# Kernel tuning notes

Hardware: AMD Instinct MI355X
Metric: run time of the kernel (lower is better)

## Reference

```python
import jax, jax.numpy as jnp
import numpy as np

N = 100000
E = 2000000
F = 64          # in_features == out_features (required by attention * h_j)
BETA = 0.5
NEG_SLOPE = 0.01  # torch F.leaky_relu default


def setup_inputs() -> dict:
    key = jax.random.key(0)
    k1, k2, k3, k4, k5, k6 = jax.random.split(key, 6)
    h = jax.random.normal(k1, (N, F), dtype=jnp.float32)
    adj = jax.random.randint(k2, (2, E), 0, N, dtype=jnp.int64)
    amount = jax.random.uniform(k3, (E,), dtype=jnp.float32)
    count = jax.random.uniform(k4, (E,), dtype=jnp.float32)
    fc_w = jax.random.normal(k5, (F, 2 * F), dtype=jnp.float32) * (1.0 / np.sqrt(2 * F))
    fc_b = jax.random.normal(k6, (F,), dtype=jnp.float32) * 0.01
    return {"h": h, "adj": adj, "amount": amount, "count": count,
            "fc_w": fc_w, "fc_b": fc_b}


def _minmax_norm(x):
    lo, hi = x.min(), x.max()
    return (x - lo) / (hi - lo + 1e-8)


def reference(h, adj, amount, count, fc_w, fc_b):
    # per-edge weight from normalized amount/count
    edge_weight = BETA * _minmax_norm(amount) + (1.0 - BETA) * _minmax_norm(count)  # [E]

    src, dst = adj[0], adj[1]
    h_i = h[src]                     # [E, F]
    h_j = h[dst]                     # [E, F]
    h_cat = jnp.concatenate([h_i, h_j], axis=1)  # [E, 2F]

    score = jnp.einsum('ef,of->eo', h_cat, fc_w) + fc_b  # [E, F_out]
    score = jnp.where(score >= 0, score, NEG_SLOPE * score)  # leaky_relu
    score = score * edge_weight[:, None]

    # softmax over ALL edges (dim 0), per feature, as in the original
    attention = jax.nn.softmax(score, axis=0)  # [E, F]

    agg = jnp.zeros_like(h).at[src].add(attention * h_j)  # scatter-add -> [N, F]
    return agg
```

## Files before the change

kernel.cpp:

```cpp
#include <hip/hip_runtime.h>
#include <hip/hip_fp16.h>
#include <math.h>

#define FDIM   64
#define NB     16
#define BSHIFT 7
#define BMASK  127
#define EPTA   16
#define CHUNKA (EPTA * 256)
#define SCH    1024
#define DMASK  0xFFFFF

__global__ __launch_bounds__(256) void count_mm_k(const int* __restrict__ src,
                                                  const float* __restrict__ amount,
                                                  const float* __restrict__ count,
                                                  int* __restrict__ mat,
                                                  float4* __restrict__ partial,
                                                  double* __restrict__ colsum,
                                                  int E, int nblkA, int nbkt) {
  __shared__ int lhist[1024];
  __shared__ float4 lred[4];
  for (int k = threadIdx.x; k < nbkt; k += 256) lhist[k] = 0;
  if (blockIdx.x == 0)
    for (int i = threadIdx.x; i < 1024; i += 256) colsum[i] = 0.0;
  __syncthreads();
  float amin = 3.4e38f, amax = -3.4e38f, cmin = 3.4e38f, cmax = -3.4e38f;
  int e0 = blockIdx.x * CHUNKA + threadIdx.x * EPTA;
  if (e0 + EPTA <= E) {
    #pragma unroll
    for (int q = 0; q < EPTA; q += 4) {
      int4   s4 = *(const int4*)(src + e0 + q);
      float4 a4 = *(const float4*)(amount + e0 + q);
      float4 c4 = *(const float4*)(count + e0 + q);
      atomicAdd(&lhist[s4.x >> BSHIFT], 1);
      atomicAdd(&lhist[s4.y >> BSHIFT], 1);
      atomicAdd(&lhist[s4.z >> BSHIFT], 1);
      atomicAdd(&lhist[s4.w >> BSHIFT], 1);
      amin = fminf(amin, fminf(fminf(a4.x, a4.y), fminf(a4.z, a4.w)));
      amax = fmaxf(amax, fmaxf(fmaxf(a4.x, a4.y), fmaxf(a4.z, a4.w)));
      cmin = fminf(cmin, fminf(fminf(c4.x, c4.y), fminf(c4.z, c4.w)));
      cmax = fmaxf(cmax, fmaxf(fmaxf(c4.x, c4.y), fmaxf(c4.z, c4.w)));
    }
  } else {
    for (int e = e0; e < E; e++) {
      atomicAdd(&lhist[src[e] >> BSHIFT], 1);
      float a = amount[e], c = count[e];
      amin = fminf(amin, a); amax = fmaxf(amax, a);
      cmin = fminf(cmin, c); cmax = fmaxf(cmax, c);
    }
  }
  #pragma unroll
  for (int off = 32; off; off >>= 1) {
    amin = fminf(amin, __shfl_down(amin, off));
    amax = fmaxf(amax, __shfl_down(amax, off));
    cmin = fminf(cmin, __shfl_down(cmin, off));
    cmax = fmaxf(cmax, __shfl_down(cmax, off));
  }
  if ((threadIdx.x & 63) == 0) lred[threadIdx.x >> 6] = make_float4(amin, amax, cmin, cmax);
  __syncthreads();
  for (int k = threadIdx.x; k < nbkt; k += 256)
    mat[(size_t)k * nblkA + blockIdx.x] = lhist[k];
  if (threadIdx.x == 0) {
    float4 r = lred[0];
    #pragma unroll
    for (int w = 1; w < 4; w++) {
      r.x = fminf(r.x, lred[w].x); r.y = fmaxf(r.y, lred[w].y);
      r.z = fminf(r.z, lred[w].z); r.w = fmaxf(r.w, lred[w].w);
    }
    partial[blockIdx.x] = r;
  }
}

__global__ __launch_bounds__(256) void scan1_k(const int* __restrict__ v,
                                               int* __restrict__ bsum, int M) {
  __shared__ int lds[256];
  int t = threadIdx.x, b = blockIdx.x;
  int s = 0;
  for (int i = b * SCH + t; i < min((b + 1) * SCH, M); i += 256) s += v[i];
  lds[t] = s; __syncthreads();
  for (int off = 128; off; off >>= 1) {
    if (t < off) lds[t] += lds[t + off];
    __syncthreads();
  }
  if (t == 0) bsum[b] = lds[0];
}

__global__ __launch_bounds__(256) void scan2_k(const int* __restrict__ bsum,
                                               int* __restrict__ bexcl, int nchunk,
                                               const float4* __restrict__ partial,
                                               float* __restrict__ mmf, int nb) {
  __shared__ int lds[256];
  int t = threadIdx.x;
  int running = 0;
  for (int c0 = 0; c0 < nchunk; c0 += 256) {
    int x = (c0 + t < nchunk) ? bsum[c0 + t] : 0;
    lds[t] = x; __syncthreads();
    for (int off = 1; off < 256; off <<= 1) {
      int v = (t >= off) ? lds[t - off] : 0;
      __syncthreads();
      lds[t] += v; __syncthreads();
    }
    if (c0 + t < nchunk) bexcl[c0 + t] = running + lds[t] - x;
    running += lds[255];
    __syncthreads();
  }
  float amin = 3.4e38f, amax = -3.4e38f, cmin = 3.4e38f, cmax = -3.4e38f;
  for (int i = t; i < nb; i += 256) {
    float4 p = partial[i];
    amin = fminf(amin, p.x); amax = fmaxf(amax, p.y);
    cmin = fminf(cmin, p.z); cmax = fmaxf(cmax, p.w);
  }
  #pragma unroll
  for (int off = 32; off; off >>= 1) {
    amin = fminf(amin, __shfl_down(amin, off));
    amax = fmaxf(amax, __shfl_down(amax, off));
    cmin = fminf(cmin, __shfl_down(cmin, off));
    cmax = fmaxf(cmax, __shfl_down(cmax, off));
  }
  __shared__ float4 lred[4];
  if ((t & 63) == 0) lred[t >> 6] = make_float4(amin, amax, cmin, cmax);
  __syncthreads();
  if (t == 0) {
    float4 r = lred[0];
    #pragma unroll
    for (int w = 1; w < 4; w++) {
      r.x = fminf(r.x, lred[w].x); r.y = fmaxf(r.y, lred[w].y);
      r.z = fminf(r.z, lred[w].z); r.w = fmaxf(r.w, lred[w].w);
    }
    mmf[0] = r.x; mmf[1] = r.y; mmf[2] = r.z; mmf[3] = r.w;
  }
}

__global__ __launch_bounds__(256) void scan3_k(const int* __restrict__ v,
                                               const int* __restrict__ bexcl,
                                               int* __restrict__ smat, int M) {
  __shared__ int lds[256];
  int t = threadIdx.x, b = blockIdx.x;
  int running = bexcl[b];
  for (int tile = 0; tile < SCH; tile += 256) {
    int i = b * SCH + tile + t;
    int x = (i < M) ? v[i] : 0;
    lds[t] = x; __syncthreads();
    for (int off = 1; off < 256; off <<= 1) {
      int vv = (t >= off) ? lds[t - off] : 0;
      __syncthreads();
      lds[t] += vv; __syncthreads();
    }
    if (i < M) smat[i] = running + lds[t] - x;
    running += lds[255];
    __syncthreads();
  }
}

__global__ __launch_bounds__(256) void scatter_k(const int* __restrict__ src,
                                                 const int* __restrict__ dst,
                                                 const float* __restrict__ amount,
                                                 const float* __restrict__ count,
                                                 const float* __restrict__ mmf,
                                                 const int* __restrict__ smat,
                                                 int2* __restrict__ payload,
                                                 int E, int nblkA, int nbkt) {
  __shared__ int cntb[1024];
  __shared__ int baseb[1024];
  __shared__ int sbase[1024];
  __shared__ int wsum[4];
  __shared__ int2 lpay[CHUNKA];
  __shared__ int lgpos[CHUNKA];
  const int t = threadIdx.x, blk = blockIdx.x;
  for (int k = t; k < nbkt; k += 256) {
    cntb[k] = 0;
    sbase[k] = smat[(size_t)k * nblkA + blk];
  }
  __syncthreads();
  const float amin = mmf[0], amax = mmf[1], cmin = mmf[2], cmax = mmf[3];
  const float L2E = 1.4426950408889634f;
  const float ascale = 0.5f * L2E / (amax - amin + 1e-8f);
  const float cscale = 0.5f * L2E / (cmax - cmin + 1e-8f);
  int e0 = blk * CHUNKA + t * EPTA;
  const bool full = (e0 + EPTA <= E);
  int4 S[4]; int4 D[4]; float4 A[4]; float4 C[4];
  if (full) {
    #pragma unroll
    for (int q = 0; q < 4; q++) {
      S[q] = *(const int4*)(src + e0 + 4 * q);
      D[q] = *(const int4*)(dst + e0 + 4 * q);
      A[q] = *(const float4*)(amount + e0 + 4 * q);
      C[q] = *(const float4*)(count + e0 + 4 * q);
      atomicAdd(&cntb[S[q].x >> BSHIFT], 1);
      atomicAdd(&cntb[S[q].y >> BSHIFT], 1);
      atomicAdd(&cntb[S[q].z >> BSHIFT], 1);
      atomicAdd(&cntb[S[q].w >> BSHIFT], 1);
    }
  } else {
    for (int e = e0; e < E; e++) atomicAdd(&cntb[src[e] >> BSHIFT], 1);
  }
  __syncthreads();
  {
    const int wv = t >> 6, ln = t & 63;
    int carry = 0;
    #pragma unroll
    for (int c = 0; c < 4; c++) {
      int idx = (wv << 8) + (c << 6) + ln;
      int x = (idx < nbkt) ? cntb[idx] : 0;
      int v = x;
      #pragma unroll
      for (int off = 1; off < 64; off <<= 1) {
        int u = __shfl_up(v, off);
        if (ln >= off) v += u;
      }
      if (idx < nbkt) baseb[idx] = carry + v - x;
      carry += __shfl(v, 63);
    }
    if (ln == 0) wsum[wv] = carry;
  }
  __syncthreads();
  {
    const int wv = t >> 6, ln = t & 63;
    int wpre = 0;
    #pragma unroll
    for (int i = 0; i < 4; i++) wpre += (i < wv) ? wsum[i] : 0;
    if (wpre) {
      #pragma unroll
      for (int c = 0; c < 4; c++) {
        int idx = (wv << 8) + (c << 6) + ln;
        if (idx < nbkt) baseb[idx] += wpre;
      }
    }
  }
  __syncthreads();
  for (int k = t; k < nbkt; k += 256) cntb[k] = baseb[k];
  __syncthreads();
  auto ins = [&](int s, int d, float a, float c) {
    int b = s >> BSHIFT;
    float ew = (a - amin) * ascale + (c - cmin) * cscale;
    int pos = atomicAdd(&cntb[b], 1);
    lpay[pos] = make_int2(d | ((s & BMASK) << 20), __float_as_int(ew));
    lgpos[pos] = sbase[b] + (pos - baseb[b]);
  };
  if (full) {
    #pragma unroll
    for (int q = 0; q < 4; q++) {
      ins(S[q].x, D[q].x, A[q].x, C[q].x);
      ins(S[q].y, D[q].y, A[q].y, C[q].y);
      ins(S[q].z, D[q].z, A[q].z, C[q].z);
      ins(S[q].w, D[q].w, A[q].w, C[q].w);
    }
  } else {
    for (int e = e0; e < E; e++) ins(src[e], dst[e], amount[e], count[e]);
  }
  __syncthreads();
  const int ned = min(CHUNKA, E - blk * CHUNKA);
  for (int i = t; i < ned; i += 256) payload[lgpos[i]] = lpay[i];
}

__global__ __launch_bounds__(256) void binB_k(const int2* __restrict__ payload,
                                              const int* __restrict__ smat,
                                              int2* __restrict__ edge_s,
                                              int E, int nblkA, int nbkt) {
  __shared__ int fcnt[128];
  __shared__ int fs[128];
  __shared__ int fcur[128];
  const int b = blockIdx.x;
  const int t = threadIdx.x;
  const int base = smat[(size_t)b * nblkA];
  const int end  = (b + 1 < nbkt) ? smat[(size_t)(b + 1) * nblkA] : E;
  if (t < 128) fcnt[t] = 0;
  __syncthreads();
  for (int i = base + t; i < end; i += 256)
    atomicAdd(&fcnt[payload[i].x >> 20], 1);
  __syncthreads();
  if (t < 128) fs[t] = fcnt[t];
  __syncthreads();
  for (int off = 1; off < 128; off <<= 1) {
    int v = 0;
    if (t < 128 && t >= off) v = fs[t - off];
    __syncthreads();
    if (t < 128) fs[t] += v;
    __syncthreads();
  }
  if (t < 128) fcur[t] = base + fs[t] - fcnt[t];
  __syncthreads();
  for (int i = base + t; i < end; i += 256) {
    int2 v = payload[i];
    int pos = atomicAdd(&fcur[v.x >> 20], 1);
    edge_s[pos] = v;
  }
}

__global__ __launch_bounds__(128) void pre_gemm(const float* __restrict__ h,
                                                const float* __restrict__ fc_w,
                                                const float* __restrict__ fc_b,
                                                float* __restrict__ G1,
                                                __half2* __restrict__ P, int N) {
  __shared__ float hs[NB * FDIM];
  const int t = threadIdx.x;
  const int o = t & 63, half = t >> 6;
  float w[FDIM];
  const float* wrow = fc_w + o * 128 + half * 64;
  #pragma unroll
  for (int f = 0; f < FDIM; f += 4) {
    float4 v = *(const float4*)(wrow + f);
    w[f] = v.x; w[f + 1] = v.y; w[f + 2] = v.z; w[f + 3] = v.w;
  }
  const float bias = (half == 0) ? fc_b[o] : 0.0f;
  const int n0 = blockIdx.x * NB;
  const int nrows = min(NB, N - n0);
  for (int i = t; i < nrows * FDIM; i += 128) hs[i] = h[(size_t)n0 * FDIM + i];
  __syncthreads();
  for (int n = 0; n < nrows; n++) {
    float acc = bias;
    #pragma unroll
    for (int f = 0; f < FDIM; f += 4) {
      float4 hv = *(const float4*)(&hs[n * FDIM + f]);
      acc += hv.x * w[f] + hv.y * w[f + 1] + hv.z * w[f + 2] + hv.w * w[f + 3];
    }
    if (half == 0) {
      G1[(size_t)(n0 + n) * FDIM + o] = acc;
    } else {
      P[(size_t)(n0 + n) * FDIM + o] =
          __halves2half2(__float2half(acc), __float2half(hs[n * FDIM + o]));
    }
  }
}

__device__ __forceinline__ float2 unpack_h2(unsigned u) {
  __half2 v = *(__half2*)&u;
  return make_float2(__low2float(v), __high2float(v));
}

__global__ __launch_bounds__(256) void fused_k(const int2* __restrict__ edge_s,
                                               const int* __restrict__ smat,
                                               const float* __restrict__ G1,
                                               const unsigned* __restrict__ P,
                                               double* __restrict__ colsum,
                                               float* __restrict__ out,
                                               int E, int nblkA, int nbkt) {
  const int lane = threadIdx.x & 63;
  const int wv = __builtin_amdgcn_readfirstlane(threadIdx.x >> 6);
  const int wid = blockIdx.x * 4 + wv;
  const int nw = gridDim.x * 4;
  float csum = 0.0f;
  const int per = (((E + nw - 1) / nw) + 63) & ~63;
  const int e0 = wid * per;
  const int e1 = min(e0 + per, E);
  if (e0 < E) {
    int lo = 0, hi = nbkt - 1;
    while (lo < hi) {
      int mid = (lo + hi + 1) >> 1;
      if (smat[(size_t)mid * nblkA] <= e0) lo = mid; else hi = mid - 1;
    }
    int bkt = lo;
    int nextb = (bkt + 1 < nbkt) ? smat[(size_t)(bkt + 1) * nblkA] : E;
    int curnode = -1;
    bool firstf = true;
    float acc = 0.0f, g1 = 0.0f;
    auto flush_to = [&](int node) {
      if (curnode >= 0) {
        float* dp = out + (size_t)curnode * FDIM + lane;
        if (firstf) { atomicAdd(dp, acc); firstf = false; }
        else *dp = acc;
      }
      curnode = node; acc = 0.0f;
      g1 = G1[(size_t)node * FDIM + lane];
    };
    for (int c0 = e0; c0 < e1; c0 += 64) {
      const int m = min(64, e1 - c0);
      int2 p = make_int2(0, 0);
      if (lane < m) p = edge_s[c0 + lane];
      if (m == 64) {
        #pragma unroll 1
        for (int j = 0; j < 64; j += 16) {
          int dd[16], nd[16]; float ee[16]; unsigned uu[16];
          #pragma unroll
          for (int k = 0; k < 16; k++) {
            int x = __builtin_amdgcn_readlane(p.x, j + k);
            ee[k] = __int_as_float(__builtin_amdgcn_readlane(p.y, j + k));
            dd[k] = x & DMASK;
            nd[k] = x >> 20;
          }
          #pragma unroll
          for (int k = 0; k < 16; k++) uu[k] = P[(size_t)dd[k] * FDIM + lane];
          #pragma unroll
          for (int k = 0; k < 16; k++) {
            int i = c0 + j + k;
            while (i >= nextb) { bkt++; nextb = (bkt + 1 < nbkt) ? smat[(size_t)(bkt + 1) * nblkA] : E; }
            int node = (bkt << BSHIFT) + nd[k];
            if (node != curnode) flush_to(node);
            float2 v = unpack_h2(uu[k]);
            float sc = g1 + v.x;
            sc = fmaxf(sc, 0.01f * sc);
            float x = exp2f(sc * ee[k]);
            csum += x;
            acc += x * v.y;
          }
        }
      } else {
        for (int j = 0; j < m; j += 16) {
          const int rem = m - j;
          int dd[16], nd[16]; float ee[16]; unsigned uu[16];
          #pragma unroll
          for (int k = 0; k < 16; k++) {
            int x = __builtin_amdgcn_readlane(p.x, j + k);
            ee[k] = __int_as_float(__builtin_amdgcn_readlane(p.y, j + k));
            dd[k] = x & DMASK;
            nd[k] = x >> 20;
          }
          #pragma unroll
          for (int k = 0; k < 16; k++) uu[k] = P[(size_t)dd[k] * FDIM + lane];
          #pragma unroll
          for (int k = 0; k < 16; k++) {
            if (k < rem) {
              int i = c0 + j + k;
              while (i >= nextb) { bkt++; nextb = (bkt + 1 < nbkt) ? smat[(size_t)(bkt + 1) * nblkA] : E; }
              int node = (bkt << BSHIFT) + nd[k];
              if (node != curnode) flush_to(node);
              float2 v = unpack_h2(uu[k]);
              float sc = g1 + v.x;
              sc = fmaxf(sc, 0.01f * sc);
              float x = exp2f(sc * ee[k]);
              csum += x;
              acc += x * v.y;
            }
          }
        }
      }
    }
    if (curnode >= 0) atomicAdd(out + (size_t)curnode * FDIM + lane, acc);
  }
  __shared__ float part[256];
  part[threadIdx.x] = csum;
  __syncthreads();
  if (threadIdx.x < 64) {
    float tot = part[threadIdx.x] + part[threadIdx.x + 64] +
                part[threadIdx.x + 128] + part[threadIdx.x + 192];
    atomicAdd(&colsum[threadIdx.x * 16], (double)tot);
  }
}

__global__ __launch_bounds__(256) void scale_k(float4* __restrict__ out4,
                                               const double* __restrict__ colsum,
                                               int total4) {
  __shared__ float rinv_s[64];
  if (threadIdx.x < 64) rinv_s[threadIdx.x] = (float)(1.0 / colsum[threadIdx.x * 16]);
  __syncthreads();
  const float4* r4 = (const float4*)rinv_s;
  int idx = blockIdx.x * blockDim.x + threadIdx.x;
  int stride = gridDim.x * blockDim.x;
  for (int i = idx; i < total4; i += stride) {
    float4 v = out4[i];
    float4 r = r4[i & 15];
    v.x *= r.x; v.y *= r.y; v.z *= r.z; v.w *= r.w;
    out4[i] = v;
  }
}

extern "C" void kernel_launch(void* const* d_in, const int* in_sizes, int n_in,
                              void* d_out, int out_size, void* d_ws, size_t ws_size,
                              hipStream_t stream) {
  const float* h      = (const float*)d_in[0];
  const int*   adj    = (const int*)d_in[1];
  const float* amount = (const float*)d_in[2];
  const float* count  = (const float*)d_in[3];
  const float* fc_w   = (const float*)d_in[4];
  const float* fc_b   = (const float*)d_in[5];
  float* out = (float*)d_out;

  const int E = in_sizes[2];
  const int N = in_sizes[0] / FDIM;
  const int* src = adj;
  const int* dst = adj + E;
  const int nbkt  = (N + BMASK) >> BSHIFT;
  const int nblkA = (E + CHUNKA - 1) / CHUNKA;
  const int M = nbkt * nblkA;
  const int nchunk = (M + SCH - 1) / SCH;

  char* ws = (char*)d_ws;
  size_t off = 0;
  auto alloc = [&](size_t bytes) { void* p = ws + off; off += (bytes + 255) & ~(size_t)255; return p; };
  float*    G1      = (float*)alloc((size_t)N * FDIM * sizeof(float));
  __half2*  P       = (__half2*)alloc((size_t)N * FDIM * sizeof(__half2));
  int2*     edge_s  = (int2*)alloc((size_t)E * sizeof(int2));
  int2*     payload = (int2*)alloc((size_t)E * sizeof(int2));
  int*      mat     = (int*)alloc((size_t)M * sizeof(int));
  int*      smat    = (int*)alloc((size_t)M * sizeof(int));
  int*      bsum    = (int*)alloc((size_t)nchunk * sizeof(int));
  int*      bexcl   = (int*)alloc((size_t)nchunk * sizeof(int));
  float4*   mmpart  = (float4*)alloc((size_t)nblkA * sizeof(float4));
  double*   colsum  = (double*)alloc(1024 * sizeof(double));
  float*    mmf     = (float*)alloc(4 * sizeof(float));

  hipMemsetAsync(d_out, 0, (size_t)out_size * sizeof(float), stream);
  count_mm_k<<<nblkA, 256, 0, stream>>>(src, amount, count, mat, mmpart, colsum, E, nblkA, nbkt);
  scan1_k<<<nchunk, 256, 0, stream>>>(mat, bsum, M);
  scan2_k<<<1, 256, 0, stream>>>(bsum, bexcl, nchunk, mmpart, mmf, nblkA);
  scan3_k<<<nchunk, 256, 0, stream>>>(mat, bexcl, smat, M);
  scatter_k<<<nblkA, 256, 0, stream>>>(src, dst, amount, count, mmf, smat, payload, E, nblkA, nbkt);
  binB_k<<<nbkt, 256, 0, stream>>>(payload, smat, edge_s, E, nblkA, nbkt);
  pre_gemm<<<(N + NB - 1) / NB, 128, 0, stream>>>(h, fc_w, fc_b, G1, P, N);
  fused_k<<<4096, 256, 0, stream>>>(edge_s, smat, G1, (const unsigned*)P, colsum, out, E, nblkA, nbkt);
  scale_k<<<1024, 256, 0, stream>>>((float4*)out, colsum, N * FDIM / 4);
}
```

Measured before the change: 306.3 us.

## Drop second-level sort; aggregate per 64-node bucket in shared-memory accumulators

Shrinks the source bucket size to 64 nodes, so each bucket's accumulators and G1 rows fit in LDS. The fine-grained per-node sort kernel (binB_k) and the output memset are removed. The fused kernel now runs one 512-thread block per bucket, accumulating with LDS atomics and writing the output once. This removes a full pass over the edge payload plus global atomics and flush logic. In exchange it adds LDS atomic contention, grows the bucket histogram to about 1563 entries, and makes per-block work depend on bucket sizes.

```diff
diff --git a/kernel.cpp b/kernel.cpp
--- a/kernel.cpp
+++ b/kernel.cpp
@@ -4,8 +4,9 @@
 
 #define FDIM   64
 #define NB     16
-#define BSHIFT 7
-#define BMASK  127
+#define BSHIFT 6
+#define BMASK  63
+#define NBKT_AL 1792
 #define EPTA   16
 #define CHUNKA (EPTA * 256)
 #define SCH    1024
@@ -18,7 +19,7 @@
                                                   float4* __restrict__ partial,
                                                   double* __restrict__ colsum,
                                                   int E, int nblkA, int nbkt) {
-  __shared__ int lhist[1024];
+  __shared__ int lhist[NBKT_AL];
   __shared__ float4 lred[4];
   for (int k = threadIdx.x; k < nbkt; k += 256) lhist[k] = 0;
   if (blockIdx.x == 0)
@@ -160,9 +161,9 @@
                                                  const int* __restrict__ smat,
                                                  int2* __restrict__ payload,
                                                  int E, int nblkA, int nbkt) {
-  __shared__ int cntb[1024];
-  __shared__ int baseb[1024];
-  __shared__ int sbase[1024];
+  __shared__ int cntb[NBKT_AL];
+  __shared__ int baseb[NBKT_AL];
+  __shared__ int sbase[NBKT_AL];
   __shared__ int wsum[4];
   __shared__ int2 lpay[CHUNKA];
   __shared__ int lgpos[CHUNKA];
@@ -199,8 +200,8 @@
     const int wv = t >> 6, ln = t & 63;
     int carry = 0;
     #pragma unroll
-    for (int c = 0; c < 4; c++) {
-      int idx = (wv << 8) + (c << 6) + ln;
+    for (int c = 0; c < 7; c++) {
+      int idx = wv * 448 + (c << 6) + ln;
       int x = (idx < nbkt) ? cntb[idx] : 0;
       int v = x;
       #pragma unroll
@@ -221,8 +222,8 @@
     for (int i = 0; i < 4; i++) wpre += (i < wv) ? wsum[i] : 0;
     if (wpre) {
       #pragma unroll
-      for (int c = 0; c < 4; c++) {
-        int idx = (wv << 8) + (c << 6) + ln;
+      for (int c = 0; c < 7; c++) {
+        int idx = wv * 448 + (c << 6) + ln;
         if (idx < nbkt) baseb[idx] += wpre;
       }
     }
@@ -251,40 +252,6 @@
   __syncthreads();
   const int ned = min(CHUNKA, E - blk * CHUNKA);
   for (int i = t; i < ned; i += 256) payload[lgpos[i]] = lpay[i];
-}
-
-__global__ __launch_bounds__(256) void binB_k(const int2* __restrict__ payload,
-                                              const int* __restrict__ smat,
-                                              int2* __restrict__ edge_s,
-                                              int E, int nblkA, int nbkt) {
-  __shared__ int fcnt[128];
-  __shared__ int fs[128];
-  __shared__ int fcur[128];
-  const int b = blockIdx.x;
-  const int t = threadIdx.x;
-  const int base = smat[(size_t)b * nblkA];
-  const int end  = (b + 1 < nbkt) ? smat[(size_t)(b + 1) * nblkA] : E;
-  if (t < 128) fcnt[t] = 0;
-  __syncthreads();
-  for (int i = base + t; i < end; i += 256)
-    atomicAdd(&fcnt[payload[i].x >> 20], 1);
-  __syncthreads();
-  if (t < 128) fs[t] = fcnt[t];
-  __syncthreads();
-  for (int off = 1; off < 128; off <<= 1) {
-    int v = 0;
-    if (t < 128 && t >= off) v = fs[t - off];
-    __syncthreads();
-    if (t < 128) fs[t] += v;
-    __syncthreads();
-  }
-  if (t < 128) fcur[t] = base + fs[t] - fcnt[t];
-  __syncthreads();
-  for (int i = base + t; i < end; i += 256) {
-    int2 v = payload[i];
-    int pos = atomicAdd(&fcur[v.x >> 20], 1);
-    edge_s[pos] = v;
-  }
 }
 
 __global__ __launch_bounds__(128) void pre_gemm(const float* __restrict__ h,
@@ -328,112 +295,97 @@
   return make_float2(__low2float(v), __high2float(v));
 }
 
-__global__ __launch_bounds__(256) void fused_k(const int2* __restrict__ edge_s,
+__global__ __launch_bounds__(512) void fused_k(const int2* __restrict__ payload,
                                                const int* __restrict__ smat,
                                                const float* __restrict__ G1,
                                                const unsigned* __restrict__ P,
                                                double* __restrict__ colsum,
                                                float* __restrict__ out,
-                                               int E, int nblkA, int nbkt) {
-  const int lane = threadIdx.x & 63;
-  const int wv = __builtin_amdgcn_readfirstlane(threadIdx.x >> 6);
-  const int wid = blockIdx.x * 4 + wv;
-  const int nw = gridDim.x * 4;
+                                               int E, int nblkA, int nbkt, int N) {
+  __shared__ float accs[64 * FDIM];
+  __shared__ float g1s[64 * FDIM];
+  __shared__ float part[512];
+  const int b = blockIdx.x;
+  const int t = threadIdx.x;
+  const int lane = t & 63;
+  const int wv = t >> 6;
+  const int node0 = b << BSHIFT;
+  const int nvalid = min(64 * FDIM, (N - node0) * FDIM);
+  for (int i = t; i < 64 * FDIM; i += 512) {
+    accs[i] = 0.0f;
+    g1s[i] = (i < nvalid) ? G1[(size_t)node0 * FDIM + i] : 0.0f;
+  }
+  const int base = smat[(size_t)b * nblkA];
+  const int end  = (b + 1 < nbkt) ? smat[(size_t)(b + 1) * nblkA] : E;
+  __syncthreads();
   float csum = 0.0f;
-  const int per = (((E + nw - 1) / nw) + 63) & ~63;
-  const int e0 = wid * per;
-  const int e1 = min(e0 + per, E);
-  if (e0 < E) {
-    int lo = 0, hi = nbkt - 1;
-    while (lo < hi) {
-      int mid = (lo + hi + 1) >> 1;
-      if (smat[(size_t)mid * nblkA] <= e0) lo = mid; else hi = mid - 1;
-    }
-    int bkt = lo;
-    int nextb = (bkt + 1 < nbkt) ? smat[(size_t)(bkt + 1) * nblkA] : E;
-    int curnode = -1;
-    bool firstf = true;
-    float acc = 0.0f, g1 = 0.0f;
-    auto flush_to = [&](int node) {
-      if (curnode >= 0) {
-        float* dp = out + (size_t)curnode * FDIM + lane;
-        if (firstf) { atomicAdd(dp, acc); firstf = false; }
-        else *dp = acc;
+  for (int c0 = base + (wv << 6); c0 < end; c0 += 512) {
+    const int m = min(64, end - c0);
+    int2 p = make_int2(0, 0);
+    if (lane < m) p = payload[c0 + lane];
+    if (m == 64) {
+      #pragma unroll 1
+      for (int j = 0; j < 64; j += 16) {
+        int xs[16]; float ee[16]; unsigned uu[16];
+        #pragma unroll
+        for (int k = 0; k < 16; k++) {
+          xs[k] = __builtin_amdgcn_readlane(p.x, j + k);
+          ee[k] = __int_as_float(__builtin_amdgcn_readlane(p.y, j + k));
+        }
+        #pragma unroll
+        for (int k = 0; k < 16; k++)
+          uu[k] = P[(size_t)(xs[k] & DMASK) * FDIM + lane];
+        __builtin_amdgcn_sched_barrier(0);
+        #pragma unroll
+        for (int k = 0; k < 16; k++) {
+          const int nd = ((unsigned)xs[k]) >> 20;
+          float g1 = g1s[(nd << 6) + lane];
+          float2 v = unpack_h2(uu[k]);
+          float sc = g1 + v.x;
+          sc = fmaxf(sc, 0.01f * sc);
+          float x = exp2f(sc * ee[k]);
+          csum += x;
+          atomicAdd(&accs[(nd << 6) + lane], x * v.y);
+        }
       }
-      curnode = node; acc = 0.0f;
-      g1 = G1[(size_t)node * FDIM + lane];
-    };
-    for (int c0 = e0; c0 < e1; c0 += 64) {
-      const int m = min(64, e1 - c0);
-      int2 p = make_int2(0, 0);
-      if (lane < m) p = edge_s[c0 + lane];
-      if (m == 64) {
-        #pragma unroll 1
-        for (int j = 0; j < 64; j += 16) {
-          int dd[16], nd[16]; float ee[16]; unsigned uu[16];
-          #pragma unroll
-          for (int k = 0; k < 16; k++) {
-            int x = __builtin_amdgcn_readlane(p.x, j + k);
-            ee[k] = __int_as_float(__builtin_amdgcn_readlane(p.y, j + k));
-            dd[k] = x & DMASK;
-            nd[k] = x >> 20;
-          }
-          #pragma unroll
-          for (int k = 0; k < 16; k++) uu[k] = P[(size_t)dd[k] * FDIM + lane];
-          #pragma unroll
-          for (int k = 0; k < 16; k++) {
-            int i = c0 + j + k;
-            while (i >= nextb) { bkt++; nextb = (bkt + 1 < nbkt) ? smat[(size_t)(bkt + 1) * nblkA] : E; }
-            int node = (bkt << BSHIFT) + nd[k];
-            if (node != curnode) flush_to(node);
+    } else {
+      for (int j = 0; j < m; j += 16) {
+        const int rem = m - j;
+        int xs[16]; float ee[16]; unsigned uu[16];
+        #pragma unroll
+        for (int k = 0; k < 16; k++) {
+          xs[k] = __builtin_amdgcn_readlane(p.x, j + k);
+          ee[k] = __int_as_float(__builtin_amdgcn_readlane(p.y, j + k));
+        }
+        #pragma unroll
+        for (int k = 0; k < 16; k++)
+          uu[k] = P[(size_t)(xs[k] & DMASK) * FDIM + lane];
+        __builtin_amdgcn_sched_barrier(0);
+        #pragma unroll
+        for (int k = 0; k < 16; k++) {
+          if (k < rem) {
+            const int nd = ((unsigned)xs[k]) >> 20;
+            float g1 = g1s[(nd << 6) + lane];
             float2 v = unpack_h2(uu[k]);
             float sc = g1 + v.x;
             sc = fmaxf(sc, 0.01f * sc);
             float x = exp2f(sc * ee[k]);
             csum += x;
-            acc += x * v.y;
-          }
-        }
-      } else {
-        for (int j = 0; j < m; j += 16) {
-          const int rem = m - j;
-          int dd[16], nd[16]; float ee[16]; unsigned uu[16];
-          #pragma unroll
-          for (int k = 0; k < 16; k++) {
-            int x = __builtin_amdgcn_readlane(p.x, j + k);
-            ee[k] = __int_as_float(__builtin_amdgcn_readlane(p.y, j + k));
-            dd[k] = x & DMASK;
-            nd[k] = x >> 20;
-          }
-          #pragma unroll
-          for (int k = 0; k < 16; k++) uu[k] = P[(size_t)dd[k] * FDIM + lane];
-          #pragma unroll
-          for (int k = 0; k < 16; k++) {
-            if (k < rem) {
-              int i = c0 + j + k;
-              while (i >= nextb) { bkt++; nextb = (bkt + 1 < nbkt) ? smat[(size_t)(bkt + 1) * nblkA] : E; }
-              int node = (bkt << BSHIFT) + nd[k];
-              if (node != curnode) flush_to(node);
-              float2 v = unpack_h2(uu[k]);
-              float sc = g1 + v.x;
-              sc = fmaxf(sc, 0.01f * sc);
-              float x = exp2f(sc * ee[k]);
-              csum += x;
-              acc += x * v.y;
-            }
+            atomicAdd(&accs[(nd << 6) + lane], x * v.y);
           }
         }
       }
     }
-    if (curnode >= 0) atomicAdd(out + (size_t)curnode * FDIM + lane, acc);
-  }
-  __shared__ float part[256];
-  part[threadIdx.x] = csum;
-  __syncthreads();
-  if (threadIdx.x < 64) {
-    float tot = part[threadIdx.x] + part[threadIdx.x + 64] +
-                part[threadIdx.x + 128] + part[threadIdx.x + 192];
-    atomicAdd(&colsum[threadIdx.x * 16], (double)tot);
+  }
+  part[t] = csum;
+  __syncthreads();
+  for (int i = t; i < nvalid; i += 512)
+    out[(size_t)node0 * FDIM + i] = accs[i];
+  if (t < FDIM) {
+    float tot = 0.0f;
+    #pragma unroll
+    for (int w = 0; w < 8; w++) tot += part[t + (w << 6)];
+    atomicAdd(&colsum[t * 16], (double)tot);
   }
 }
 
@@ -479,7 +431,6 @@
   auto alloc = [&](size_t bytes) { void* p = ws + off; off += (bytes + 255) & ~(size_t)255; return p; };
   float*    G1      = (float*)alloc((size_t)N * FDIM * sizeof(float));
   __half2*  P       = (__half2*)alloc((size_t)N * FDIM * sizeof(__half2));
-  int2*     edge_s  = (int2*)alloc((size_t)E * sizeof(int2));
   int2*     payload = (int2*)alloc((size_t)E * sizeof(int2));
   int*      mat     = (int*)alloc((size_t)M * sizeof(int));
   int*      smat    = (int*)alloc((size_t)M * sizeof(int));
@@ -489,14 +440,12 @@
   double*   colsum  = (double*)alloc(1024 * sizeof(double));
   float*    mmf     = (float*)alloc(4 * sizeof(float));
 
-  hipMemsetAsync(d_out, 0, (size_t)out_size * sizeof(float), stream);
   count_mm_k<<<nblkA, 256, 0, stream>>>(src, amount, count, mat, mmpart, colsum, E, nblkA, nbkt);
   scan1_k<<<nchunk, 256, 0, stream>>>(mat, bsum, M);
   scan2_k<<<1, 256, 0, stream>>>(bsum, bexcl, nchunk, mmpart, mmf, nblkA);
   scan3_k<<<nchunk, 256, 0, stream>>>(mat, bexcl, smat, M);
   scatter_k<<<nblkA, 256, 0, stream>>>(src, dst, amount, count, mmf, smat, payload, E, nblkA, nbkt);
-  binB_k<<<nbkt, 256, 0, stream>>>(payload, smat, edge_s, E, nblkA, nbkt);
   pre_gemm<<<(N + NB - 1) / NB, 128, 0, stream>>>(h, fc_w, fc_b, G1, P, N);
-  fused_k<<<4096, 256, 0, stream>>>(edge_s, smat, G1, (const unsigned*)P, colsum, out, E, nblkA, nbkt);
+  fused_k<<<nbkt, 512, 0, stream>>>(payload, smat, G1, (const unsigned*)P, colsum, out, E, nblkA, nbkt, N);
   scale_k<<<1024, 256, 0, stream>>>((float4*)out, colsum, N * FDIM / 4);
 }
```

New measurement: 939.2 us. 3.07x slower.

## Double-buffer edge gathers in the aggregation loop to overlap loads with compute

Applied to the files above, without the earlier changes.

Replaces the 64-edge chunk loop, which loaded edges coalesced and broadcast them with readlane, with a software-pipelined loop over groups of 16 edges. Each group's edge records are read directly as uniform loads and its P rows gathered into one register set while the previous group is being computed from the other set. A scalar tail loop handles the leftover edges. This hides gather latency behind the exp/accumulate work, at the cost of roughly doubled register use for the staging arrays, which may reduce occupancy.

```diff
diff --git a/kernel.cpp b/kernel.cpp
--- a/kernel.cpp
+++ b/kernel.cpp
@@ -363,67 +363,69 @@
       curnode = node; acc = 0.0f;
       g1 = G1[(size_t)node * FDIM + lane];
     };
-    for (int c0 = e0; c0 < e1; c0 += 64) {
-      const int m = min(64, e1 - c0);
-      int2 p = make_int2(0, 0);
-      if (lane < m) p = edge_s[c0 + lane];
-      if (m == 64) {
-        #pragma unroll 1
-        for (int j = 0; j < 64; j += 16) {
-          int dd[16], nd[16]; float ee[16]; unsigned uu[16];
-          #pragma unroll
-          for (int k = 0; k < 16; k++) {
-            int x = __builtin_amdgcn_readlane(p.x, j + k);
-            ee[k] = __int_as_float(__builtin_amdgcn_readlane(p.y, j + k));
-            dd[k] = x & DMASK;
-            nd[k] = x >> 20;
-          }
-          #pragma unroll
-          for (int k = 0; k < 16; k++) uu[k] = P[(size_t)dd[k] * FDIM + lane];
-          #pragma unroll
-          for (int k = 0; k < 16; k++) {
-            int i = c0 + j + k;
-            while (i >= nextb) { bkt++; nextb = (bkt + 1 < nbkt) ? smat[(size_t)(bkt + 1) * nblkA] : E; }
-            int node = (bkt << BSHIFT) + nd[k];
-            if (node != curnode) flush_to(node);
-            float2 v = unpack_h2(uu[k]);
-            float sc = g1 + v.x;
-            sc = fmaxf(sc, 0.01f * sc);
-            float x = exp2f(sc * ee[k]);
-            csum += x;
-            acc += x * v.y;
-          }
+    auto stage16 = [&](int b0, int* xs, float* ee, unsigned* uu) {
+      #pragma unroll
+      for (int k = 0; k < 16; k++) {
+        int2 q = edge_s[b0 + k];
+        xs[k] = q.x;
+        ee[k] = __int_as_float(q.y);
+      }
+      #pragma unroll
+      for (int k = 0; k < 16; k++)
+        uu[k] = P[(size_t)(xs[k] & DMASK) * FDIM + lane];
+    };
+    auto compute16 = [&](const int* xs, const float* ee, const unsigned* uu,
+                         int i0) {
+      #pragma unroll
+      for (int k = 0; k < 16; k++) {
+        int i = i0 + k;
+        while (i >= nextb) { bkt++; nextb = (bkt + 1 < nbkt) ? smat[(size_t)(bkt + 1) * nblkA] : E; }
+        int node = (bkt << BSHIFT) + (((unsigned)xs[k]) >> 20);
+        if (node != curnode) flush_to(node);
+        float2 v = unpack_h2(uu[k]);
+        float sc = g1 + v.x;
+        sc = fmaxf(sc, 0.01f * sc);
+        float x = exp2f(sc * ee[k]);
+        csum += x;
+        acc += x * v.y;
+      }
+    };
+    const int nfull = (e1 - e0) >> 4;
+    const int rem = (e1 - e0) & 15;
+    int xsA[16], xsB[16];
+    float eeA[16], eeB[16];
+    unsigned uuA[16], uuB[16];
+    int i = 0;
+    if (nfull > 0) {
+      stage16(e0, xsA, eeA, uuA);
+      while (i + 2 <= nfull) {
+        stage16(e0 + (i + 1) * 16, xsB, eeB, uuB);
+        compute16(xsA, eeA, uuA, e0 + i * 16);
+        if (i + 2 < nfull) {
+          stage16(e0 + (i + 2) * 16, xsA, eeA, uuA);
+          compute16(xsB, eeB, uuB, e0 + (i + 1) * 16);
+        } else {
+          compute16(xsB, eeB, uuB, e0 + (i + 1) * 16);
         }
-      } else {
-        for (int j = 0; j < m; j += 16) {
-          const int rem = m - j;
-          int dd[16], nd[16]; float ee[16]; unsigned uu[16];
-          #pragma unroll
-          for (int k = 0; k < 16; k++) {
-            int x = __builtin_amdgcn_readlane(p.x, j + k);
-            ee[k] = __int_as_float(__builtin_amdgcn_readlane(p.y, j + k));
-            dd[k] = x & DMASK;
-            nd[k] = x >> 20;
-          }
-          #pragma unroll
-          for (int k = 0; k < 16; k++) uu[k] = P[(size_t)dd[k] * FDIM + lane];
-          #pragma unroll
-          for (int k = 0; k < 16; k++) {
-            if (k < rem) {
-              int i = c0 + j + k;
-              while (i >= nextb) { bkt++; nextb = (bkt + 1 < nbkt) ? smat[(size_t)(bkt + 1) * nblkA] : E; }
-              int node = (bkt << BSHIFT) + nd[k];
-              if (node != curnode) flush_to(node);
-              float2 v = unpack_h2(uu[k]);
-              float sc = g1 + v.x;
-              sc = fmaxf(sc, 0.01f * sc);
-              float x = exp2f(sc * ee[k]);
-              csum += x;
-              acc += x * v.y;
-            }
-          }
-        }
+        i += 2;
       }
+      if (i < nfull)
+        compute16(xsA, eeA, uuA, e0 + i * 16);
+    }
+    int b0 = e0 + nfull * 16;
+    for (int t2 = 0; t2 < rem; t2++) {
+      int2 q = edge_s[b0 + t2];
+      unsigned u = P[(size_t)(q.x & DMASK) * FDIM + lane];
+      int ii = b0 + t2;
+      while (ii >= nextb) { bkt++; nextb = (bkt + 1 < nbkt) ? smat[(size_t)(bkt + 1) * nblkA] : E; }
+      int node = (bkt << BSHIFT) + (((unsigned)q.x) >> 20);
+      if (node != curnode) flush_to(node);
+      float2 v = unpack_h2(u);
+      float sc = g1 + v.x;
+      sc = fmaxf(sc, 0.01f * sc);
+      float x = exp2f(sc * __int_as_float(q.y));
+      csum += x;
+      acc += x * v.y;
     }
     if (curnode >= 0) atomicAdd(out + (size_t)curnode * FDIM + lane, acc);
   }
```

Result: no change. 309.9 us (+1.2%).
